# Kernel optimization log

Hardware: AMD Instinct MI355X
Metric: run time of the kernel (lower is better)

Reference implementation:

```python
import jax, jax.numpy as jnp
import numpy as np

B, C, H, W = 4, 128, 64, 64
NUM_HEADS = 4
EPS = 1e-5


def setup_inputs() -> dict:
    key = jax.random.key(0)
    k1, k2, k3 = jax.random.split(key, 3)
    x = jax.random.normal(k1, (B, C, H, W), dtype=jnp.float32)
    gn_w = jnp.ones((C,), jnp.float32)
    gn_b = jnp.zeros((C,), jnp.float32)
    qkv_w = 0.02 * jax.random.normal(k2, (3 * C, C), dtype=jnp.float32)
    qkv_b = jnp.zeros((3 * C,), jnp.float32)
    proj_w = 0.02 * jax.random.normal(k3, (C, C), dtype=jnp.float32)
    proj_b = jnp.zeros((C,), jnp.float32)
    return {"x": x, "gn_w": gn_w, "gn_b": gn_b, "qkv_w": qkv_w,
            "qkv_b": qkv_b, "proj_w": proj_w, "proj_b": proj_b}


def reference(x, gn_w, gn_b, qkv_w, qkv_b, proj_w, proj_b):
    b, c, h, w = x.shape
    nh = NUM_HEADS
    dh = c // nh
    hw = h * w
    # GroupNorm with 1 group: normalize over (C,H,W) per sample, biased var
    mean = jnp.mean(x, axis=(1, 2, 3), keepdims=True)
    var = jnp.var(x, axis=(1, 2, 3), keepdims=True)
    xn = (x - mean) * jax.lax.rsqrt(var + EPS)
    xn = xn * gn_w[None, :, None, None] + gn_b[None, :, None, None]
    # 1x1 conv == channel matmul: (b,c,h,w) -> (b,3c,h,w)
    qkv = jnp.einsum('bchw,oc->bohw', xn, qkv_w) + qkv_b[None, :, None, None]
    qkv = qkv.reshape(b, 3, nh, dh, hw)
    q, k, v = qkv[:, 0], qkv[:, 1], qkv[:, 2]  # each (b, nh, dh, hw)
    scale = dh ** (-0.5)
    # attn: (b, nh, hw, hw)
    attn = jax.nn.softmax(jnp.einsum('bhdn,bhdm->bhnm', q, k) * scale, axis=-1)
    out = jnp.einsum('bhnm,bhdm->bhnd', attn, v)  # (b, nh, hw, dh)
    # faithful to torch: permute(0,3,1,2) -> (b, dh, nh, hw), then reshape(b,c,h,w)
    out = jnp.transpose(out, (0, 3, 1, 2)).reshape(b, c, h, w)
    out = jnp.einsum('bchw,oc->bohw', out, proj_w) + proj_b[None, :, None, None]
    return out + x
```

## Files before the change

### kernel.cpp

```cpp
#include <hip/hip_runtime.h>
#include <math.h>

#define HW 4096
#define CH 128
#define NH 4
#define DH 32

typedef unsigned short u16;
typedef __attribute__((ext_vector_type(8))) short bf16x8;
typedef __attribute__((ext_vector_type(4))) float f32x4;
typedef __attribute__((ext_vector_type(16))) float f32x16;
typedef __attribute__((ext_vector_type(4))) unsigned short u16x4;
typedef __attribute__((ext_vector_type(8))) unsigned short u16x8;

#if __has_builtin(__builtin_amdgcn_exp2f)
#define KFOLD (0.17677669529663687f * 1.4426950408889634f)
#define FASTEXP(x) __builtin_amdgcn_exp2f(x)
#else
#define KFOLD 0.17677669529663687f
#define FASTEXP(x) __expf(x)
#endif

#if __has_builtin(__builtin_amdgcn_rcpf)
#define RCPF(x) __builtin_amdgcn_rcpf(x)
#else
#define RCPF(x) (1.f / (x))
#endif

__device__ __forceinline__ u16 f2bf(float f) {
    union { float f; unsigned u; } a; a.f = f;
    unsigned u = a.u;
    unsigned r = u + 0x7FFFu + ((u >> 16) & 1u);
    return (u16)(r >> 16);
}
__device__ __forceinline__ float bf2f(u16 u) {
    union { unsigned u; float f; } a; a.u = ((unsigned)u) << 16;
    return a.f;
}
__device__ __forceinline__ unsigned pack2bf_t(float a, float b) {
    union { float f; unsigned u; } ua, ub; ua.f = a; ub.f = b;
    return __builtin_amdgcn_perm(ub.u, ua.u, 0x07060302u);
}

__global__ __launch_bounds__(256) void prep_kernel(
    const float* __restrict__ x, float* __restrict__ partials,
    const float* __restrict__ qkv_w, const float* __restrict__ proj_w,
    u16* __restrict__ wq, u16* __restrict__ wp) {
    int blk = blockIdx.x, t = threadIdx.x;
    if (blk < 512) {
        const float4* xv = (const float4*)(x + (size_t)blk * 4096);
        float s = 0.f, sq = 0.f;
#pragma unroll
        for (int i = 0; i < 4; ++i) {
            float4 v = xv[t + 256 * i];
            s  += v.x + v.y + v.z + v.w;
            sq += v.x * v.x + v.y * v.y + v.z * v.z + v.w * v.w;
        }
#pragma unroll
        for (int off = 32; off > 0; off >>= 1) {
            s  += __shfl_down(s, off, 64);
            sq += __shfl_down(sq, off, 64);
        }
        __shared__ float red[8];
        int wave = t >> 6, lane = t & 63;
        if (lane == 0) { red[wave * 2] = s; red[wave * 2 + 1] = sq; }
        __syncthreads();
        if (t == 0) {
            partials[blk * 2]     = red[0] + red[2] + red[4] + red[6];
            partials[blk * 2 + 1] = red[1] + red[3] + red[5] + red[7];
        }
    } else {
        int i = (blk - 512) * 256 + t;
        if (i < 49152) wq[i] = f2bf(qkv_w[i]);
        else           wp[i - 49152] = f2bf(proj_w[i - 49152]);
    }
}

__global__ __launch_bounds__(256) void qkv_mfma_kernel(
    const float* __restrict__ x, const float* __restrict__ gn_w, const float* __restrict__ gn_b,
    const u16* __restrict__ wq, const float* __restrict__ qkv_b, const float* __restrict__ partials,
    u16* __restrict__ qo, u16* __restrict__ ko, u16* __restrict__ vo) {
    __shared__ u16 xt[32 * 136];
    __shared__ float sstats[2];
    int b = blockIdx.y, p0 = blockIdx.x * 32, t = threadIdx.x;
    const float* xb = x + (size_t)b * CH * HW;
    float4 xv[4]; int cc[4], pp[4];
#pragma unroll
    for (int i = 0; i < 4; ++i) {
        int u = t + 256 * i;
        cc[i] = u >> 3; pp[i] = (u & 7) * 4;
        xv[i] = *(const float4*)&xb[(size_t)cc[i] * HW + p0 + pp[i]];
    }
    if (t < 64) {
        float s  = partials[(b * 128 + t) * 2]     + partials[(b * 128 + 64 + t) * 2];
        float sq = partials[(b * 128 + t) * 2 + 1] + partials[(b * 128 + 64 + t) * 2 + 1];
#pragma unroll
        for (int off = 32; off > 0; off >>= 1) {
            s  += __shfl_down(s, off, 64);
            sq += __shfl_down(sq, off, 64);
        }
        if (t == 0) {
            const float invN = 1.f / (float)(CH * HW);
            float mean = s * invN;
            float var  = sq * invN - mean * mean;
            sstats[0] = mean;
            sstats[1] = rsqrtf(var + 1e-5f);
        }
    }
    __syncthreads();
    float mean = sstats[0], rstd = sstats[1];
#pragma unroll
    for (int i = 0; i < 4; ++i) {
        float sc = rstd * gn_w[cc[i]], bb = gn_b[cc[i]] - mean * sc;
        xt[(pp[i] + 0) * 136 + cc[i]] = f2bf(fmaf(xv[i].x, sc, bb));
        xt[(pp[i] + 1) * 136 + cc[i]] = f2bf(fmaf(xv[i].y, sc, bb));
        xt[(pp[i] + 2) * 136 + cc[i]] = f2bf(fmaf(xv[i].z, sc, bb));
        xt[(pp[i] + 3) * 136 + cc[i]] = f2bf(fmaf(xv[i].w, sc, bb));
    }
    __syncthreads();
    int wave = t >> 6, lane = t & 63, l16 = lane & 15, quad = lane >> 4;
    f32x4 acc[6][2];
#pragma unroll
    for (int os = 0; os < 6; ++os)
#pragma unroll
        for (int ps = 0; ps < 2; ++ps) acc[os][ps] = f32x4{0.f, 0.f, 0.f, 0.f};
#pragma unroll
    for (int kc = 0; kc < 4; ++kc) {
        bf16x8 bfr[2];
#pragma unroll
        for (int ps = 0; ps < 2; ++ps)
            bfr[ps] = *(const bf16x8*)&xt[(ps * 16 + l16) * 136 + kc * 32 + quad * 8];
#pragma unroll
        for (int os = 0; os < 6; ++os) {
            bf16x8 af = *(const bf16x8*)&wq[(size_t)(wave * 96 + os * 16 + l16) * 128 + kc * 32 + quad * 8];
#pragma unroll
            for (int ps = 0; ps < 2; ++ps)
                acc[os][ps] = __builtin_amdgcn_mfma_f32_16x16x32_bf16(af, bfr[ps], acc[os][ps], 0, 0, 0);
        }
    }
#pragma unroll
    for (int os = 0; os < 6; ++os) {
        int obase = wave * 96 + os * 16 + quad * 4;
        int sec = obase >> 7;
        if (sec == 2) continue;
        float4 bias = *(const float4*)&qkv_b[obase];
        int oc = obase & 127, h = oc >> 5, d = oc & 31;
        float km = (sec == 1) ? KFOLD : 1.f;
#pragma unroll
        for (int ps = 0; ps < 2; ++ps) {
            int p = p0 + ps * 16 + l16;
            u16x4 pk = {f2bf((acc[os][ps][0] + bias.x) * km),
                        f2bf((acc[os][ps][1] + bias.y) * km),
                        f2bf((acc[os][ps][2] + bias.z) * km),
                        f2bf((acc[os][ps][3] + bias.w) * km)};
            *(u16x4*)((sec == 0 ? qo : ko) + ((size_t)(b * NH + h) * HW + p) * DH + d) = pk;
        }
    }
    __syncthreads();
    u16* vt = xt;
    int l16p2 = (l16 & 3) | ((l16 & 4) << 1) | ((l16 & 8) >> 1);
#pragma unroll
    for (int os = 0; os < 6; ++os) {
        int obase = wave * 96 + os * 16 + quad * 4;
        if ((obase >> 7) != 2) continue;
        float4 bias = *(const float4*)&qkv_b[obase];
        int oc = obase & 127;
#pragma unroll
        for (int ps = 0; ps < 2; ++ps) {
            int colm = ps * 16 + l16p2;
            vt[(oc + 0) * 34 + colm] = f2bf(acc[os][ps][0] + bias.x);
            vt[(oc + 1) * 34 + colm] = f2bf(acc[os][ps][1] + bias.y);
            vt[(oc + 2) * 34 + colm] = f2bf(acc[os][ps][2] + bias.z);
            vt[(oc + 3) * 34 + colm] = f2bf(acc[os][ps][3] + bias.w);
        }
    }
    __syncthreads();
#pragma unroll
    for (int i = 0; i < 2; ++i) {
        int row = i * 64 + (t >> 2), colv = (t & 3) * 8;
        *(u16x8*)&vo[((size_t)b * CH + row) * HW + p0 + colv] = *(const u16x8*)&vt[row * 34 + colv];
    }
}

__global__ __launch_bounds__(256, 4) void attn_mfma_kernel(
    const u16* __restrict__ q, const u16* __restrict__ k, const u16* __restrict__ v,
    u16* __restrict__ Op, float* __restrict__ lp) {
    __shared__ u16 smem[16384];
    int bh = blockIdx.z, mpart = blockIdx.y, t = threadIdx.x;
    int wave = t >> 6, lane = t & 63, l31 = lane & 31, hf = lane >> 5;
    const u16* qb = q + (size_t)bh * HW * DH;
    const u16* kb = k + (size_t)bh * HW * DH;
    const u16* vb = v + (size_t)bh * DH * HW;
    int n_g = blockIdx.x * 128 + wave * 32 + l31;
    int m_base = mpart * 2048;

    bf16x8 bq0 = *(const bf16x8*)&qb[(size_t)n_g * DH + hf * 8];
    bf16x8 bq1 = *(const bf16x8*)&qb[(size_t)n_g * DH + 16 + hf * 8];

    int km_ = t >> 2, kg_ = t & 3;
    int kswz_w = (kg_ ^ (km_ & 3) ^ ((km_ >> 2) & 1)) * 8;
    int kw0 = km_ * 32 + kswz_w, kw1 = (km_ + 64) * 32 + kswz_w;
    const u16* kgp = kb + (size_t)(m_base + km_) * DH + kg_ * 8;
    int vd_ = t >> 3, vg_ = t & 7;
    int vswz = (vg_ ^ (vd_ & 7)) * 8;
    int vw0 = vd_ * 128 + vswz, vw1 = vd_ * 128 + 64 + vswz;
    const u16* vgp = vb + (size_t)vd_ * HW + m_base + vg_ * 8;

    int kswz_r = (l31 & 3) ^ ((l31 >> 2) & 1);
    int kro[2][2], vro[4];
#pragma unroll
    for (int ms = 0; ms < 2; ++ms)
#pragma unroll
        for (int kc = 0; kc < 2; ++kc)
            kro[ms][kc] = (ms * 32 + l31) * 32 + (((2 * kc + hf) ^ kswz_r) * 8);
#pragma unroll
    for (int kc = 0; kc < 4; ++kc)
        vro[kc] = l31 * 128 + (((2 * kc + hf) ^ (l31 & 7)) * 8);

    const f32x16 zero16 = {0.f,0.f,0.f,0.f,0.f,0.f,0.f,0.f,0.f,0.f,0.f,0.f,0.f,0.f,0.f,0.f};
    f32x16 accO = zero16;
    float l_part = 0.f;

    bf16x8 kregA = *(const bf16x8*)kgp;
    bf16x8 kregB = *(const bf16x8*)(kgp + 64 * DH);
    bf16x8 vregA = *(const bf16x8*)vgp;
    bf16x8 vregB = *(const bf16x8*)(vgp + 64);

    for (int it = 0; it < 16; ++it) {
        u16* Ksb = smem + (it & 1) * 4096;
        u16* Vsb = smem + 8192 + (it & 1) * 4096;
        *(bf16x8*)&Ksb[kw0] = kregA;
        *(bf16x8*)&Ksb[kw1] = kregB;
        *(bf16x8*)&Vsb[vw0] = vregA;
        *(bf16x8*)&Vsb[vw1] = vregB;
        __syncthreads();
        if (it < 15) {
            const u16* kp = kgp + (size_t)(it + 1) * 128 * DH;
            kregA = *(const bf16x8*)kp;
            kregB = *(const bf16x8*)(kp + 64 * DH);
            const u16* vp = vgp + (it + 1) * 128;
            vregA = *(const bf16x8*)vp;
            vregB = *(const bf16x8*)(vp + 64);
        }
#pragma unroll
        for (int h = 0; h < 2; ++h) {
            const u16* Kh = Ksb + h * 2048;
            f32x16 s0, s1;
            {
                bf16x8 a00 = *(const bf16x8*)&Kh[kro[0][0]];
                bf16x8 a01 = *(const bf16x8*)&Kh[kro[0][1]];
                s0 = __builtin_amdgcn_mfma_f32_32x32x16_bf16(a00, bq0, zero16, 0, 0, 0);
                s0 = __builtin_amdgcn_mfma_f32_32x32x16_bf16(a01, bq1, s0, 0, 0, 0);
                bf16x8 a10 = *(const bf16x8*)&Kh[kro[1][0]];
                bf16x8 a11 = *(const bf16x8*)&Kh[kro[1][1]];
                s1 = __builtin_amdgcn_mfma_f32_32x32x16_bf16(a10, bq0, zero16, 0, 0, 0);
                s1 = __builtin_amdgcn_mfma_f32_32x32x16_bf16(a11, bq1, s1, 0, 0, 0);
            }
            unsigned pk[2][8];
#pragma unroll
            for (int qq = 0; qq < 8; ++qq) {
                float e0 = FASTEXP(s0[2 * qq]), e1 = FASTEXP(s0[2 * qq + 1]);
                l_part += e0 + e1;
                pk[0][qq] = pack2bf_t(e0, e1);
                float f0 = FASTEXP(s1[2 * qq]), f1 = FASTEXP(s1[2 * qq + 1]);
                l_part += f0 + f1;
                pk[1][qq] = pack2bf_t(f0, f1);
            }
#pragma unroll
            for (int kc = 0; kc < 4; ++kc) {
                int ms = kc >> 1, Qb = 4 * (kc & 1);
                union { unsigned u[4]; bf16x8 v; } bu;
                bu.u[0] = pk[ms][Qb + 0];
                bu.u[1] = pk[ms][Qb + 1];
                bu.u[2] = pk[ms][Qb + 2];
                bu.u[3] = pk[ms][Qb + 3];
                bf16x8 av = *(const bf16x8*)&Vsb[vro[kc] + h * 64];
                accO = __builtin_amdgcn_mfma_f32_32x32x16_bf16(av, bu.v, accO, 0, 0, 0);
            }
        }
    }
    l_part += __shfl_xor(l_part, 32, 64);
    if (hf == 0) lp[((size_t)bh * HW + n_g) * 2 + mpart] = l_part;
    __syncthreads();
    u16* tb = smem;
    int nloc = wave * 32 + l31;
#pragma unroll
    for (int r = 0; r < 16; ++r) {
        int d = (r & 3) + 8 * (r >> 2) + 4 * hf;
        tb[nloc * 36 + d] = f2bf(accO[r]);
    }
    __syncthreads();
    size_t obase = ((size_t)(mpart * 16 + bh) * HW + blockIdx.x * 128) * 32;
#pragma unroll
    for (int i = 0; i < 2; ++i) {
        int row = i * 64 + (t >> 2), col = (t & 3) * 8;
        *(u16x8*)&Op[obase + (size_t)row * 32 + col] = *(const u16x8*)&tb[row * 36 + col];
    }
}

__global__ __launch_bounds__(256) void proj_mfma_kernel(
    const u16* __restrict__ Op, const float* __restrict__ lp,
    const u16* __restrict__ wp, const float* __restrict__ proj_b,
    const float* __restrict__ x, float* __restrict__ out) {
    __shared__ u16 at_t[32 * 136];
    int b = blockIdx.y, p0 = blockIdx.x * 32, t = threadIdx.x;
#pragma unroll
    for (int i = 0; i < 2; ++i) {
        int u = t + 256 * i;
        int p = u >> 4, hh = (u >> 2) & 3, ch = u & 3;
        int bh = b * NH + hh;
        size_t nidx = (size_t)bh * HW + p0 + p;
        float2 l2 = *(const float2*)&lp[nidx * 2];
        float lsum = l2.x + l2.y;
        float sum8[8] = {0.f,0.f,0.f,0.f,0.f,0.f,0.f,0.f};
#pragma unroll
        for (int part = 0; part < 2; ++part) {
            u16x8 ov = *(const u16x8*)&Op[((size_t)(part * 16 + bh) * HW + p0 + p) * 32 + ch * 8];
#pragma unroll
            for (int j = 0; j < 8; ++j) sum8[j] += bf2f(ov[j]);
        }
        float rin = RCPF(lsum);
#pragma unroll
        for (int j = 0; j < 8; ++j)
            at_t[p * 136 + (ch * 8 + j) * 4 + hh] = f2bf(sum8[j] * rin);
    }
    __syncthreads();
    int wave = t >> 6, lane = t & 63, l16 = lane & 15, quad = lane >> 4;
    f32x4 acc[2][2];
#pragma unroll
    for (int os = 0; os < 2; ++os)
#pragma unroll
        for (int ps = 0; ps < 2; ++ps) acc[os][ps] = f32x4{0.f, 0.f, 0.f, 0.f};
#pragma unroll
    for (int kc = 0; kc < 4; ++kc) {
        bf16x8 bfr[2];
#pragma unroll
        for (int ps = 0; ps < 2; ++ps)
            bfr[ps] = *(const bf16x8*)&at_t[(ps * 16 + l16) * 136 + kc * 32 + quad * 8];
#pragma unroll
        for (int os = 0; os < 2; ++os) {
            bf16x8 af = *(const bf16x8*)&wp[(size_t)(wave * 32 + os * 16 + l16) * 128 + kc * 32 + quad * 8];
#pragma unroll
            for (int ps = 0; ps < 2; ++ps)
                acc[os][ps] = __builtin_amdgcn_mfma_f32_16x16x32_bf16(af, bfr[ps], acc[os][ps], 0, 0, 0);
        }
    }
#pragma unroll
    for (int os = 0; os < 2; ++os) {
        int obase = wave * 32 + os * 16 + quad * 4;
#pragma unroll
        for (int ps = 0; ps < 2; ++ps) {
            int p = p0 + ps * 16 + l16;
#pragma unroll
            for (int r = 0; r < 4; ++r) {
                size_t idx = ((size_t)b * CH + obase + r) * HW + p;
                out[idx] = acc[os][ps][r] + proj_b[obase + r] + x[idx];
            }
        }
    }
}

extern "C" void kernel_launch(void* const* d_in, const int* in_sizes, int n_in,
                              void* d_out, int out_size, void* d_ws, size_t ws_size,
                              hipStream_t stream) {
    const float* x      = (const float*)d_in[0];
    const float* gn_w   = (const float*)d_in[1];
    const float* gn_b   = (const float*)d_in[2];
    const float* qkv_w  = (const float*)d_in[3];
    const float* qkv_b  = (const float*)d_in[4];
    const float* proj_w = (const float*)d_in[5];
    const float* proj_b = (const float*)d_in[6];
    float* out = (float*)d_out;

    char* W = (char*)d_ws;
    float* partials = (float*)(W + 0);
    u16*   wq       = (u16*)(W + 8192);
    u16*   wp       = (u16*)(W + 8192 + 98304);
    u16*   qo       = (u16*)(W + 139264);
    u16*   ko       = qo + (size_t)2097152;
    u16*   vo       = ko + (size_t)2097152;
    u16*   Op       = vo + (size_t)2097152;
    float* lp       = (float*)(Op + (size_t)2 * 2097152);

    hipLaunchKernelGGL(prep_kernel,      dim3(768),       dim3(256), 0, stream,
                       x, partials, qkv_w, proj_w, wq, wp);
    hipLaunchKernelGGL(qkv_mfma_kernel,  dim3(128, 4),    dim3(256), 0, stream,
                       x, gn_w, gn_b, wq, qkv_b, partials, qo, ko, vo);
    hipLaunchKernelGGL(attn_mfma_kernel, dim3(32, 2, 16), dim3(256), 0, stream,
                       qo, ko, vo, Op, lp);
    hipLaunchKernelGGL(proj_mfma_kernel, dim3(128, 4),    dim3(256), 0, stream,
                       Op, lp, wp, proj_b, x, out);
}
```

Measured before the change: 143.7 us.

## Pre-swizzle weights into MFMA fragment order and pad attention LDS tiles

The weight-conversion prologue now writes qkv and proj weights in per-wave MFMA fragment order, so each lane's 16-byte A-fragment load becomes fully contiguous across the wavefront instead of strided by rows. Separately, the attention kernel drops the XOR swizzle for K/V shared-memory tiles and uses padded row strides (36 and 132 elements) to avoid bank conflicts. The padding enlarges LDS use per block, which could affect occupancy at 4 blocks per CU. Padded layouts may also misalign 16-byte LDS accesses or leave some bank conflicts.

Measured after the change: 228.7 us. 59.2% more time.

```diff
diff --git a/kernel.cpp b/kernel.cpp
--- a/kernel.cpp
+++ b/kernel.cpp
@@ -71,8 +71,22 @@
         }
     } else {
         int i = (blk - 512) * 256 + t;
-        if (i < 49152) wq[i] = f2bf(qkv_w[i]);
-        else           wp[i - 49152] = f2bf(proj_w[i - 49152]);
+        if (i < 49152) {
+            int dstBlk = i >> 9, lane = (i >> 3) & 63, j = i & 7;
+            int wave = dstBlk / 24, rem = dstBlk % 24;
+            int os = rem >> 2, kc = rem & 3;
+            int o = wave * 96 + os * 16 + (lane & 15);
+            int c = kc * 32 + (lane >> 4) * 8 + j;
+            wq[i] = f2bf(qkv_w[o * 128 + c]);
+        } else {
+            int i2 = i - 49152;
+            int dstBlk = i2 >> 9, lane = (i2 >> 3) & 63, j = i2 & 7;
+            int wave = dstBlk >> 3, rem = dstBlk & 7;
+            int os = rem >> 2, kc = rem & 3;
+            int o = wave * 32 + os * 16 + (lane & 15);
+            int c = kc * 32 + (lane >> 4) * 8 + j;
+            wp[i2] = f2bf(proj_w[o * 128 + c]);
+        }
     }
 }
 
@@ -132,7 +146,7 @@
             bfr[ps] = *(const bf16x8*)&xt[(ps * 16 + l16) * 136 + kc * 32 + quad * 8];
 #pragma unroll
         for (int os = 0; os < 6; ++os) {
-            bf16x8 af = *(const bf16x8*)&wq[(size_t)(wave * 96 + os * 16 + l16) * 128 + kc * 32 + quad * 8];
+            bf16x8 af = *(const bf16x8*)&wq[((wave * 6 + os) * 4 + kc) * 512 + lane * 8];
 #pragma unroll
             for (int ps = 0; ps < 2; ++ps)
                 acc[os][ps] = __builtin_amdgcn_mfma_f32_16x16x32_bf16(af, bfr[ps], acc[os][ps], 0, 0, 0);
@@ -185,7 +199,7 @@
 __global__ __launch_bounds__(256, 4) void attn_mfma_kernel(
     const u16* __restrict__ q, const u16* __restrict__ k, const u16* __restrict__ v,
     u16* __restrict__ Op, float* __restrict__ lp) {
-    __shared__ u16 smem[16384];
+    __shared__ u16 smem[17664];
     int bh = blockIdx.z, mpart = blockIdx.y, t = threadIdx.x;
     int wave = t >> 6, lane = t & 63, l31 = lane & 31, hf = lane >> 5;
     const u16* qb = q + (size_t)bh * HW * DH;
@@ -198,24 +212,21 @@
     bf16x8 bq1 = *(const bf16x8*)&qb[(size_t)n_g * DH + 16 + hf * 8];
 
     int km_ = t >> 2, kg_ = t & 3;
-    int kswz_w = (kg_ ^ (km_ & 3) ^ ((km_ >> 2) & 1)) * 8;
-    int kw0 = km_ * 32 + kswz_w, kw1 = (km_ + 64) * 32 + kswz_w;
+    int kw0 = km_ * 36 + kg_ * 8, kw1 = kw0 + 64 * 36;
     const u16* kgp = kb + (size_t)(m_base + km_) * DH + kg_ * 8;
     int vd_ = t >> 3, vg_ = t & 7;
-    int vswz = (vg_ ^ (vd_ & 7)) * 8;
-    int vw0 = vd_ * 128 + vswz, vw1 = vd_ * 128 + 64 + vswz;
+    int vw0 = vd_ * 132 + vg_ * 8, vw1 = vw0 + 64;
     const u16* vgp = vb + (size_t)vd_ * HW + m_base + vg_ * 8;
 
-    int kswz_r = (l31 & 3) ^ ((l31 >> 2) & 1);
     int kro[2][2], vro[4];
 #pragma unroll
     for (int ms = 0; ms < 2; ++ms)
 #pragma unroll
         for (int kc = 0; kc < 2; ++kc)
-            kro[ms][kc] = (ms * 32 + l31) * 32 + (((2 * kc + hf) ^ kswz_r) * 8);
+            kro[ms][kc] = (ms * 32 + l31) * 36 + (2 * kc + hf) * 8;
 #pragma unroll
     for (int kc = 0; kc < 4; ++kc)
-        vro[kc] = l31 * 128 + (((2 * kc + hf) ^ (l31 & 7)) * 8);
+        vro[kc] = l31 * 132 + (2 * kc + hf) * 8;
 
     const f32x16 zero16 = {0.f,0.f,0.f,0.f,0.f,0.f,0.f,0.f,0.f,0.f,0.f,0.f,0.f,0.f,0.f,0.f};
     f32x16 accO = zero16;
@@ -227,8 +238,8 @@
     bf16x8 vregB = *(const bf16x8*)(vgp + 64);
 
     for (int it = 0; it < 16; ++it) {
-        u16* Ksb = smem + (it & 1) * 4096;
-        u16* Vsb = smem + 8192 + (it & 1) * 4096;
+        u16* Ksb = smem + (it & 1) * 4608;
+        u16* Vsb = smem + 9216 + (it & 1) * 4224;
         *(bf16x8*)&Ksb[kw0] = kregA;
         *(bf16x8*)&Ksb[kw1] = kregB;
         *(bf16x8*)&Vsb[vw0] = vregA;
@@ -244,7 +255,7 @@
         }
 #pragma unroll
         for (int h = 0; h < 2; ++h) {
-            const u16* Kh = Ksb + h * 2048;
+            const u16* Kh = Ksb + h * 2304;
             f32x16 s0, s1;
             {
                 bf16x8 a00 = *(const bf16x8*)&Kh[kro[0][0]];
@@ -339,7 +350,7 @@
             bfr[ps] = *(const bf16x8*)&at_t[(ps * 16 + l16) * 136 + kc * 32 + quad * 8];
 #pragma unroll
         for (int os = 0; os < 2; ++os) {
-            bf16x8 af = *(const bf16x8*)&wp[(size_t)(wave * 32 + os * 16 + l16) * 128 + kc * 32 + quad * 8];
+            bf16x8 af = *(const bf16x8*)&wp[((wave * 2 + os) * 4 + kc) * 512 + lane * 8];
 #pragma unroll
             for (int ps = 0; ps < 2; ++ps)
                 acc[os][ps] = __builtin_amdgcn_mfma_f32_16x16x32_bf16(af, bfr[ps], acc[os][ps], 0, 0, 0);
```
